# Kernel tuning notes

Hardware: AMD Instinct MI355X
Metric: run time of the kernel (lower is better)

Reference implementation:

```python
import jax, jax.numpy as jnp
import numpy as np

N = 50000          # num_nodes
E = 800000         # general (base) edge count
R_BASE = 3         # base relation types
R = 2 * R_BASE + 1 # base + inverse + self-loop relation
D_IN = 64
D_HID = 64
D_OUT = 64


def _glorot(k, shape):
    # xavier_uniform with relu gain, fan over last two dims
    gain = np.sqrt(2.0)
    bound = gain * np.sqrt(6.0 / (shape[-2] + shape[-1]))
    return jax.random.uniform(k, shape, jnp.float32, -bound, bound)


def setup_inputs() -> dict:
    key = jax.random.key(0)
    ks = jax.random.split(key, 6)
    x = jax.random.normal(ks[0], (N, D_IN), dtype=jnp.float32)
    src = jax.random.randint(ks[1], (E,), 0, N)
    dst = jax.random.randint(ks[2], (E,), 0, N)
    et = jax.random.randint(ks[3], (E,), 0, R_BASE)
    nodes = jnp.arange(N)
    # triples = [original edges, inverse edges (type+R_BASE), self-loops (type 2*R_BASE)]
    triples = jnp.concatenate([
        jnp.stack([src, et, dst], axis=1),
        jnp.stack([dst, et + R_BASE, src], axis=1),
        jnp.stack([nodes, jnp.full((N,), 2 * R_BASE), nodes], axis=1),
    ], axis=0).astype(jnp.int64)
    w1 = _glorot(ks[4], (R, D_IN, D_HID))
    w2 = _glorot(ks[5], (R, D_HID, D_OUT))
    b1 = jnp.zeros((D_HID,), jnp.float32)
    b2 = jnp.zeros((D_OUT,), jnp.float32)
    return {"x": x, "w1": w1, "b1": b1, "w2": w2, "b2": b2,
            "triples": triples, "num_nodes": N, "num_edge_types": R}


def _rgcn_layer(x, W, b, triples, num_nodes, num_rels):
    # vertical stacking: sparse adj [R*N, N], entry (r*N+src, dst) = 1, row-normalised
    src, et, dst = triples[:, 0], triples[:, 1], triples[:, 2]
    rows = et * num_nodes + src                     # [T] row index in stacked adj
    counts = jnp.zeros((num_rels * num_nodes,), x.dtype).at[rows].add(1.0)
    vals = 1.0 / counts[rows]                       # per-edge row-normalised weight
    msgs = vals[:, None] * x[dst]                   # [T, d] gathered + scaled messages
    af = jax.ops.segment_sum(msgs, rows, num_segments=num_rels * num_nodes)
    af = af.reshape(num_rels, num_nodes, x.shape[1])  # [R, N, d]
    return jnp.einsum('rio,rni->no', W, af) + b


def reference(x, w1, b1, w2, b2, triples, num_nodes, num_edge_types):
    h = _rgcn_layer(x, w1, b1, triples, num_nodes, num_edge_types)
    h = jax.nn.relu(h)
    out = _rgcn_layer(h, w2, b2, triples, num_nodes, num_edge_types)
    return out
```

## Files before the change

kernel.cpp:

```cpp
#include <hip/hip_runtime.h>
#include <stdint.h>

#define D 64
#define TILE 2048
#define PK 8
#define NBMAX 128
#define BW 512
#define RMAX 8

typedef __attribute__((ext_vector_type(8))) short bf16x8;
typedef __attribute__((ext_vector_type(4))) float f32x4;

__device__ __forceinline__ float bf2f(unsigned short u) {
    union { unsigned int i; float f; } v; v.i = ((unsigned int)u) << 16; return v.f;
}
__device__ __forceinline__ unsigned short f2bf(float f) {
    union { float f; unsigned int i; } v; v.f = f;
    unsigned int x = v.i;
    unsigned int r = (x + 0x7FFFu + ((x >> 16) & 1u)) >> 16;
    return (unsigned short)r;
}
__device__ __forceinline__ float lo_bf(unsigned int u) {
    union { unsigned int i; float f; } v; v.i = u << 16; return v.f;
}
__device__ __forceinline__ float hi_bf(unsigned int u) {
    union { unsigned int i; float f; } v; v.i = u & 0xFFFF0000u; return v.f;
}

__global__ void detect_kernel(const int* __restrict__ t32, int probe, int expect,
                              unsigned int* __restrict__ flag) {
    if (blockIdx.x == 0 && threadIdx.x == 0)
        flag[0] = (t32[probe] == expect) ? 0u : 1u;
}

__global__ void __launch_bounds__(256) binpass_kernel(const unsigned int* __restrict__ t32,
                                                      const unsigned int* __restrict__ flag,
                                                      unsigned int* __restrict__ staging,
                                                      unsigned int* __restrict__ binCnt,
                                                      int M, int NB, int CAP) {
    __shared__ unsigned int sorted[TILE];
    __shared__ unsigned char sortedb[TILE];
    __shared__ unsigned int hist[NBMAX];
    __shared__ unsigned int scan_[NBMAX];
    __shared__ unsigned int cur[NBMAX];
    __shared__ unsigned int gbase[NBMAX];

    int tid = threadIdx.x;
    int tileBase = blockIdx.x * TILE;

    for (int i = tid; i < NBMAX; i += 256) hist[i] = 0;
    __syncthreads();

    bool is64 = flag[0] != 0;
    unsigned int myE[PK];
    unsigned char myB[PK];
    #pragma unroll
    for (int k = 0; k < PK; k++) {
        int e = tileBase + tid * PK + k;
        myB[k] = 0xFF;
        if (e < M) {
            long w = (long)e * 3;
            unsigned int src, et, dst;
            if (is64) { src = t32[2*w]; et = t32[2*(w+1)]; dst = t32[2*(w+2)]; }
            else      { src = t32[w];   et = t32[w+1];     dst = t32[w+2]; }
            unsigned int b = src >> 9;
            unsigned int lsrc = src & (BW - 1);
            myE[k] = (lsrc << 20) | (et << 17) | dst;
            myB[k] = (unsigned char)b;
            atomicAdd(&hist[b], 1u);
        }
    }
    __syncthreads();

    if (tid < NBMAX) scan_[tid] = hist[tid];
    __syncthreads();
    for (int off = 1; off < NBMAX; off <<= 1) {
        unsigned int v = (tid < NBMAX && tid >= off) ? scan_[tid - off] : 0u;
        __syncthreads();
        if (tid < NBMAX) scan_[tid] += v;
        __syncthreads();
    }
    if (tid < NB) {
        gbase[tid] = atomicAdd(&binCnt[tid], hist[tid]);
        cur[tid] = scan_[tid] - hist[tid];
    }
    __syncthreads();

    #pragma unroll
    for (int k = 0; k < PK; k++) {
        if (myB[k] != 0xFF) {
            unsigned int p = atomicAdd(&cur[myB[k]], 1u);
            sorted[p] = myE[k];
            sortedb[p] = myB[k];
        }
    }
    __syncthreads();

    unsigned int total = scan_[NB - 1];
    for (unsigned int i = tid; i < total; i += 256) {
        unsigned int b = sortedb[i];
        unsigned int local = i - (scan_[b] - hist[b]);
        unsigned int slot = gbase[b] + local;
        if (slot < (unsigned int)CAP)
            staging[(size_t)b * CAP + slot] = sorted[i];
    }
}

__global__ void __launch_bounds__(512) buildcsr_kernel(const unsigned int* __restrict__ staging,
                                                       const unsigned int* __restrict__ binCnt,
                                                       unsigned int* __restrict__ offsets,
                                                       uint2* __restrict__ adj,
                                                       int M, int N, int R, int NB, int CAP) {
    __shared__ unsigned int hist7[RMAX * BW];
    __shared__ unsigned int scanbuf[BW];
    __shared__ unsigned int curs[BW];
    __shared__ unsigned int sbase[NBMAX];

    int b = blockIdx.x, tid = threadIdx.x;
    int nodeBase = b * BW;
    int nNodes = N - nodeBase; if (nNodes > BW) nNodes = BW;
    unsigned int cntB = binCnt[b]; if (cntB > (unsigned int)CAP) cntB = CAP;

    for (int i = tid; i < RMAX * BW; i += 512) hist7[i] = 0;
    __syncthreads();

    const unsigned int* st = staging + (size_t)b * CAP;
    for (unsigned int i = tid; i < cntB; i += 512) {
        unsigned int e = st[i];
        unsigned int lsrc = e >> 20, et = (e >> 17) & 7u;
        atomicAdd(&hist7[et * BW + lsrc], 1u);
    }
    __syncthreads();

    unsigned int d = 0;
    for (int r2 = 0; r2 < R; r2++) d += hist7[r2 * BW + tid];
    scanbuf[tid] = d;
    __syncthreads();
    for (int off = 1; off < BW; off <<= 1) {
        unsigned int v = (tid >= off) ? scanbuf[tid - off] : 0u;
        __syncthreads();
        scanbuf[tid] += v;
        __syncthreads();
    }

    if (tid < NBMAX) sbase[tid] = (tid < NB) ? min(binCnt[tid], (unsigned int)CAP) : 0u;
    __syncthreads();
    for (int off = 1; off < NBMAX; off <<= 1) {
        unsigned int v = (tid < NBMAX && tid >= off) ? sbase[tid - off] : 0u;
        __syncthreads();
        if (tid < NBMAX) sbase[tid] += v;
        __syncthreads();
    }
    unsigned int baseB = (b == 0) ? 0u : sbase[b - 1];

    unsigned int nodeStart = baseB + scanbuf[tid] - d;
    if (tid < nNodes) offsets[nodeBase + tid] = nodeStart;
    if (b == NB - 1 && tid == 0) offsets[N] = baseB + cntB;
    curs[tid] = nodeStart;
    __syncthreads();

    for (unsigned int i = tid; i < cntB; i += 512) {
        unsigned int e = st[i];
        unsigned int lsrc = e >> 20, et = (e >> 17) & 7u, dst = e & 0x1FFFFu;
        unsigned int pos = atomicAdd(&curs[lsrc], 1u);
        float val = 1.0f / (float)hist7[et * BW + lsrc];
        uint2 m; m.x = dst * (unsigned int)R + et; m.y = __float_as_uint(val);
        adj[pos] = m;
    }
}

__global__ void convert_kernel(const float* __restrict__ x, unsigned short* __restrict__ xb, int total) {
    int i = (blockIdx.x * blockDim.x + threadIdx.x) * 4;
    if (i + 3 < total) {
        float4 v = *(const float4*)(x + i);
        ushort4 o; o.x = f2bf(v.x); o.y = f2bf(v.y); o.z = f2bf(v.z); o.w = f2bf(v.w);
        *(ushort4*)(xb + i) = o;
    } else {
        for (int j = i; j < total; j++) xb[j] = f2bf(x[j]);
    }
}

__global__ void packw_kernel(const float* __restrict__ W, unsigned short* __restrict__ wpack, int R) {
    int gid = blockIdx.x * blockDim.x + threadIdx.x;
    if (gid >= R * 512) return;
    int lane = gid & 63;
    int c = (gid >> 6) & 3;
    int t = (gid >> 8) & 1;
    int r = gid >> 9;
    int col = c * 16 + (lane & 15);
    int kbase = t * 32 + 8 * (lane >> 4);
    #pragma unroll
    for (int j = 0; j < 8; j++) {
        wpack[(size_t)gid * 8 + j] = f2bf(W[((size_t)r * D + kbase + j) * D + col]);
    }
}

__global__ void __launch_bounds__(256) gemm_mfma_kernel(const unsigned short* __restrict__ xb,
                                                        const unsigned short* __restrict__ wpack,
                                                        unsigned short* __restrict__ y,
                                                        int N, int R, int nchunks) {
    int wid = blockIdx.x * 4 + (threadIdx.x >> 6);
    int lane = threadIdx.x & 63;
    if (wid >= R * nchunks) return;
    int r = wid / nchunks;
    int chunk = wid - r * nchunks;
    int n0 = chunk * 16;

    int arow = n0 + (lane & 15);
    if (arow >= N) arow = N - 1;
    const unsigned short* xr = xb + (size_t)arow * D + 8 * (lane >> 4);
    bf16x8 a0 = *(const bf16x8*)(xr);
    bf16x8 a1 = *(const bf16x8*)(xr + 32);

    const unsigned short* wp = wpack + (size_t)r * 4096 + (size_t)lane * 8;
    f32x4 zero = {0.f, 0.f, 0.f, 0.f};

    int colb = lane & 15;
    int rowbase = n0 + (lane >> 4) * 4;
    #pragma unroll
    for (int c = 0; c < 4; c++) {
        bf16x8 b0 = *(const bf16x8*)(wp + (size_t)(c) * 512);
        bf16x8 b1 = *(const bf16x8*)(wp + (size_t)(4 + c) * 512);
        f32x4 acc = __builtin_amdgcn_mfma_f32_16x16x32_bf16(a0, b0, zero, 0, 0, 0);
        acc       = __builtin_amdgcn_mfma_f32_16x16x32_bf16(a1, b1, acc,  0, 0, 0);
        int col = 16 * c + colb;
        #pragma unroll
        for (int q = 0; q < 4; q++) {
            int row = rowbase + q;
            if (row < N) y[((size_t)row * R + r) * D + col] = f2bf(acc[q]);
        }
    }
}

__global__ void __launch_bounds__(256) gather_kernel(const unsigned short* __restrict__ y,
                                                     const uint2* __restrict__ adj,
                                                     const unsigned int* __restrict__ offsets,
                                                     const float* __restrict__ bias,
                                                     unsigned int* __restrict__ out_bf,
                                                     float* __restrict__ out_f32,
                                                     int N, int totalWaves, int mode) {
    int w = blockIdx.x * 4 + (threadIdx.x >> 6);
    int lane = threadIdx.x & 63;
    int h = lane >> 5;
    int c = lane & 31;
    float2 bl = ((const float2*)bias)[c];

    for (int n = w; n < N; n += totalWaves) {
        int nu = __builtin_amdgcn_readfirstlane(n);
        unsigned int s = offsets[nu], e = offsets[nu + 1];
        float acc0 = 0.f, acc1 = 0.f;
        unsigned int np = (e - s) >> 1;
        #pragma unroll 4
        for (unsigned int it = 0; it < np; ++it) {
            unsigned int eidx = s + 2 * it + h;
            uint2 m = adj[eidx];
            unsigned int u = *(const unsigned int*)(y + (size_t)m.x * D + 2 * c);
            float val = __uint_as_float(m.y);
            acc0 += val * lo_bf(u);
            acc1 += val * hi_bf(u);
        }
        if ((e - s) & 1u) {
            uint2 m = adj[e - 1];
            unsigned int u = *(const unsigned int*)(y + (size_t)m.x * D + 2 * c);
            float val = (h == 0) ? __uint_as_float(m.y) : 0.f;
            acc0 += val * lo_bf(u);
            acc1 += val * hi_bf(u);
        }
        acc0 += __shfl_xor(acc0, 32);
        acc1 += __shfl_xor(acc1, 32);
        if (lane < 32) {
            float o0 = acc0 + bl.x;
            float o1 = acc1 + bl.y;
            if (mode == 0) {
                o0 = fmaxf(o0, 0.f); o1 = fmaxf(o1, 0.f);
                out_bf[(size_t)nu * 32 + c] =
                    ((unsigned int)f2bf(o1) << 16) | (unsigned int)f2bf(o0);
            } else {
                ((float2*)out_f32)[(size_t)nu * 32 + c] = make_float2(o0, o1);
            }
        }
    }
}

extern "C" void kernel_launch(void* const* d_in, const int* in_sizes, int n_in,
                              void* d_out, int out_size, void* d_ws, size_t ws_size,
                              hipStream_t stream) {
    const float* x  = (const float*)d_in[0];
    const float* w1 = (const float*)d_in[1];
    const float* b1 = (const float*)d_in[2];
    const float* w2 = (const float*)d_in[3];
    const float* b2 = (const float*)d_in[4];
    const int* trip = (const int*)d_in[5];

    const int N = in_sizes[0] / D;
    const int R = in_sizes[1] / (D * D);
    const int M = in_sizes[5] / 3;

    const int NB = (N + BW - 1) / BW;
    const int CAP = (((2 * (M / NB)) + 1023) / 1024) * 1024;

    char* p = (char*)d_ws;
    auto alloc = [&](size_t bytes) { void* q = (void*)p; p += (bytes + 255) / 256 * 256; return q; };
    unsigned int* binCnt  = (unsigned int*)alloc((size_t)NBMAX * 4);
    unsigned int* offsets = (unsigned int*)alloc(((size_t)N + 1) * 4);
    unsigned int* flag    = (unsigned int*)alloc(256);
    unsigned int* staging = (unsigned int*)alloc((size_t)NB * CAP * 4);
    uint2*        adj     = (uint2*)alloc((size_t)M * 8);
    unsigned short* ybf   = (unsigned short*)alloc((size_t)N * R * D * 2);
    unsigned short* xb    = (unsigned short*)alloc((size_t)N * D * 2);
    unsigned short* hb    = (unsigned short*)alloc((size_t)N * D * 2);
    unsigned short* wp1   = (unsigned short*)alloc((size_t)R * 512 * 8 * 2);
    unsigned short* wp2   = (unsigned short*)alloc((size_t)R * 512 * 8 * 2);

    hipMemsetAsync(binCnt, 0, (size_t)NBMAX * 4, stream);

    int probe = (M - N) * 3 + 1;
    detect_kernel<<<1, 1, 0, stream>>>(trip, probe, R - 1, flag);

    int tiles = (M + TILE - 1) / TILE;
    binpass_kernel<<<tiles, 256, 0, stream>>>((const unsigned int*)trip, flag, staging, binCnt, M, NB, CAP);
    buildcsr_kernel<<<NB, 512, 0, stream>>>(staging, binCnt, offsets, adj, M, N, R, NB, CAP);

    int totX = N * D;
    convert_kernel<<<(totX / 4 + 255) / 256, 256, 0, stream>>>(x, xb, totX);
    packw_kernel<<<(R * 512 + 255) / 256, 256, 0, stream>>>(w1, wp1, R);
    packw_kernel<<<(R * 512 + 255) / 256, 256, 0, stream>>>(w2, wp2, R);

    int nchunks = (N + 15) / 16;
    int gb = (R * nchunks + 3) / 4;
    int gblocks = 2048, tw = gblocks * 4;

    gemm_mfma_kernel<<<gb, 256, 0, stream>>>(xb, wp1, ybf, N, R, nchunks);
    gather_kernel<<<gblocks, 256, 0, stream>>>(ybf, adj, offsets, b1, (unsigned int*)hb, nullptr, N, tw, 0);
    gemm_mfma_kernel<<<gb, 256, 0, stream>>>(hb, wp2, ybf, N, R, nchunks);
    gather_kernel<<<gblocks, 256, 0, stream>>>(ybf, adj, offsets, b2, nullptr, (float*)d_out, N, tw, 1);
}
```

Baseline: 272.8 us.

## Aggregate per relation first, then apply a single concatenated-K MFMA GEMM

Reorders each layer from transform-then-gather to aggregate-then-transform. The CSR is now segmented per node and relation, and a new agg kernel gathers raw 64-wide bf16 features into a per-relation concatenated buffer. The self-loop relation is served straight from the feature table. A fused GEMM with K=448 then applies all relation weights, bias and ReLU at once. This removes the N×R×64 intermediate write and the gather from that larger table, in exchange for serial per-relation segment loops with small segments, a wider afcat write and reread, and higher register use in the GEMM.

```diff
diff --git a/kernel.cpp b/kernel.cpp
--- a/kernel.cpp
+++ b/kernel.cpp
@@ -11,9 +11,6 @@
 typedef __attribute__((ext_vector_type(8))) short bf16x8;
 typedef __attribute__((ext_vector_type(4))) float f32x4;
 
-__device__ __forceinline__ float bf2f(unsigned short u) {
-    union { unsigned int i; float f; } v; v.i = ((unsigned int)u) << 16; return v.f;
-}
 __device__ __forceinline__ unsigned short f2bf(float f) {
     union { float f; unsigned int i; } v; v.f = f;
     unsigned int x = v.i;
@@ -108,12 +105,12 @@
 
 __global__ void __launch_bounds__(512) buildcsr_kernel(const unsigned int* __restrict__ staging,
                                                        const unsigned int* __restrict__ binCnt,
-                                                       unsigned int* __restrict__ offsets,
+                                                       unsigned int* __restrict__ segOff,
                                                        uint2* __restrict__ adj,
                                                        int M, int N, int R, int NB, int CAP) {
     __shared__ unsigned int hist7[RMAX * BW];
+    __shared__ unsigned int curs7[RMAX * BW];
     __shared__ unsigned int scanbuf[BW];
-    __shared__ unsigned int curs[BW];
     __shared__ unsigned int sbase[NBMAX];
 
     int b = blockIdx.x, tid = threadIdx.x;
@@ -154,17 +151,25 @@
     unsigned int baseB = (b == 0) ? 0u : sbase[b - 1];
 
     unsigned int nodeStart = baseB + scanbuf[tid] - d;
-    if (tid < nNodes) offsets[nodeBase + tid] = nodeStart;
-    if (b == NB - 1 && tid == 0) offsets[N] = baseB + cntB;
-    curs[tid] = nodeStart;
+    if (tid < nNodes) {
+        unsigned int o = nodeStart;
+        for (int et = 0; et < R; et++) {
+            segOff[(size_t)(nodeBase + tid) * 8 + et] = o;
+            curs7[et * BW + tid] = o;
+            o += hist7[et * BW + tid];
+        }
+        segOff[(size_t)(nodeBase + tid) * 8 + R] = o;
+    } else {
+        for (int et = 0; et < R; et++) curs7[et * BW + tid] = 0;
+    }
     __syncthreads();
 
     for (unsigned int i = tid; i < cntB; i += 512) {
         unsigned int e = st[i];
         unsigned int lsrc = e >> 20, et = (e >> 17) & 7u, dst = e & 0x1FFFFu;
-        unsigned int pos = atomicAdd(&curs[lsrc], 1u);
+        unsigned int pos = atomicAdd(&curs7[et * BW + lsrc], 1u);
         float val = 1.0f / (float)hist7[et * BW + lsrc];
-        uint2 m; m.x = dst * (unsigned int)R + et; m.y = __float_as_uint(val);
+        uint2 m; m.x = dst; m.y = __float_as_uint(val);
         adj[pos] = m;
     }
 }
@@ -195,88 +200,90 @@
     }
 }
 
-__global__ void __launch_bounds__(256) gemm_mfma_kernel(const unsigned short* __restrict__ xb,
-                                                        const unsigned short* __restrict__ wpack,
-                                                        unsigned short* __restrict__ y,
-                                                        int N, int R, int nchunks) {
-    int wid = blockIdx.x * 4 + (threadIdx.x >> 6);
-    int lane = threadIdx.x & 63;
-    if (wid >= R * nchunks) return;
-    int r = wid / nchunks;
-    int chunk = wid - r * nchunks;
-    int n0 = chunk * 16;
-
-    int arow = n0 + (lane & 15);
-    if (arow >= N) arow = N - 1;
-    const unsigned short* xr = xb + (size_t)arow * D + 8 * (lane >> 4);
-    bf16x8 a0 = *(const bf16x8*)(xr);
-    bf16x8 a1 = *(const bf16x8*)(xr + 32);
-
-    const unsigned short* wp = wpack + (size_t)r * 4096 + (size_t)lane * 8;
-    f32x4 zero = {0.f, 0.f, 0.f, 0.f};
-
-    int colb = lane & 15;
-    int rowbase = n0 + (lane >> 4) * 4;
-    #pragma unroll
-    for (int c = 0; c < 4; c++) {
-        bf16x8 b0 = *(const bf16x8*)(wp + (size_t)(c) * 512);
-        bf16x8 b1 = *(const bf16x8*)(wp + (size_t)(4 + c) * 512);
-        f32x4 acc = __builtin_amdgcn_mfma_f32_16x16x32_bf16(a0, b0, zero, 0, 0, 0);
-        acc       = __builtin_amdgcn_mfma_f32_16x16x32_bf16(a1, b1, acc,  0, 0, 0);
-        int col = 16 * c + colb;
-        #pragma unroll
-        for (int q = 0; q < 4; q++) {
-            int row = rowbase + q;
-            if (row < N) y[((size_t)row * R + r) * D + col] = f2bf(acc[q]);
-        }
-    }
-}
-
-__global__ void __launch_bounds__(256) gather_kernel(const unsigned short* __restrict__ y,
-                                                     const uint2* __restrict__ adj,
-                                                     const unsigned int* __restrict__ offsets,
-                                                     const float* __restrict__ bias,
-                                                     unsigned int* __restrict__ out_bf,
-                                                     float* __restrict__ out_f32,
-                                                     int N, int totalWaves, int mode) {
+__global__ void __launch_bounds__(256) agg_kernel(const unsigned short* __restrict__ xtab,
+                                                  const uint2* __restrict__ adj,
+                                                  const unsigned int* __restrict__ segOff,
+                                                  unsigned int* __restrict__ afcat,
+                                                  int N, int totalWaves, int Rm1) {
     int w = blockIdx.x * 4 + (threadIdx.x >> 6);
     int lane = threadIdx.x & 63;
     int h = lane >> 5;
     int c = lane & 31;
-    float2 bl = ((const float2*)bias)[c];
+    int stride = Rm1 * 32;
 
     for (int n = w; n < N; n += totalWaves) {
         int nu = __builtin_amdgcn_readfirstlane(n);
-        unsigned int s = offsets[nu], e = offsets[nu + 1];
-        float acc0 = 0.f, acc1 = 0.f;
-        unsigned int np = (e - s) >> 1;
-        #pragma unroll 4
-        for (unsigned int it = 0; it < np; ++it) {
-            unsigned int eidx = s + 2 * it + h;
-            uint2 m = adj[eidx];
-            unsigned int u = *(const unsigned int*)(y + (size_t)m.x * D + 2 * c);
-            float val = __uint_as_float(m.y);
-            acc0 += val * lo_bf(u);
-            acc1 += val * hi_bf(u);
-        }
-        if ((e - s) & 1u) {
-            uint2 m = adj[e - 1];
-            unsigned int u = *(const unsigned int*)(y + (size_t)m.x * D + 2 * c);
-            float val = (h == 0) ? __uint_as_float(m.y) : 0.f;
-            acc0 += val * lo_bf(u);
-            acc1 += val * hi_bf(u);
-        }
-        acc0 += __shfl_xor(acc0, 32);
-        acc1 += __shfl_xor(acc1, 32);
-        if (lane < 32) {
-            float o0 = acc0 + bl.x;
-            float o1 = acc1 + bl.y;
-            if (mode == 0) {
-                o0 = fmaxf(o0, 0.f); o1 = fmaxf(o1, 0.f);
-                out_bf[(size_t)nu * 32 + c] =
-                    ((unsigned int)f2bf(o1) << 16) | (unsigned int)f2bf(o0);
-            } else {
-                ((float2*)out_f32)[(size_t)nu * 32 + c] = make_float2(o0, o1);
+        for (int r = 0; r < Rm1; r++) {
+            unsigned int s = segOff[(size_t)nu * 8 + r], e = segOff[(size_t)nu * 8 + r + 1];
+            float acc0 = 0.f, acc1 = 0.f;
+            unsigned int cnt = e - s;
+            unsigned int np = cnt >> 1;
+            for (unsigned int it = 0; it < np; ++it) {
+                uint2 m = adj[s + 2 * it + h];
+                unsigned int u = *(const unsigned int*)(xtab + (size_t)m.x * D + 2 * c);
+                float val = __uint_as_float(m.y);
+                acc0 += val * lo_bf(u);
+                acc1 += val * hi_bf(u);
+            }
+            if (cnt & 1u) {
+                uint2 m = adj[e - 1];
+                unsigned int u = *(const unsigned int*)(xtab + (size_t)m.x * D + 2 * c);
+                float val = (h == 0) ? __uint_as_float(m.y) : 0.f;
+                acc0 += val * lo_bf(u);
+                acc1 += val * hi_bf(u);
+            }
+            acc0 += __shfl_xor(acc0, 32);
+            acc1 += __shfl_xor(acc1, 32);
+            if (lane < 32)
+                afcat[(size_t)nu * stride + r * 32 + c] =
+                    ((unsigned int)f2bf(acc1) << 16) | (unsigned int)f2bf(acc0);
+        }
+    }
+}
+
+__global__ void __launch_bounds__(256) gemm2_kernel(const unsigned short* __restrict__ afcat,
+                                                    const unsigned short* __restrict__ xtab,
+                                                    const unsigned short* __restrict__ wpack,
+                                                    const float* __restrict__ bias,
+                                                    unsigned short* __restrict__ out_bf,
+                                                    float* __restrict__ out_f32,
+                                                    int N, int nchunks, int mode) {
+    int wid = blockIdx.x * 4 + (threadIdx.x >> 6);
+    int lane = threadIdx.x & 63;
+    if (wid >= nchunks) return;
+    int n0 = wid * 16;
+    int arow = n0 + (lane & 15);
+    if (arow >= N) arow = N - 1;
+    int ksub = 8 * (lane >> 4);
+
+    bf16x8 a[14];
+    const unsigned short* af = afcat + (size_t)arow * 384 + ksub;
+    #pragma unroll
+    for (int kt = 0; kt < 12; kt++) a[kt] = *(const bf16x8*)(af + kt * 32);
+    const unsigned short* xr = xtab + (size_t)arow * D + ksub;
+    a[12] = *(const bf16x8*)(xr);
+    a[13] = *(const bf16x8*)(xr + 32);
+
+    const unsigned short* wp = wpack + (size_t)lane * 8;
+    int colb = lane & 15;
+    int rowbase = n0 + (lane >> 4) * 4;
+    #pragma unroll
+    for (int c = 0; c < 4; c++) {
+        f32x4 acc = {0.f, 0.f, 0.f, 0.f};
+        #pragma unroll
+        for (int kt = 0; kt < 14; kt++) {
+            bf16x8 bfr = *(const bf16x8*)(wp + (size_t)(kt * 4 + c) * 512);
+            acc = __builtin_amdgcn_mfma_f32_16x16x32_bf16(a[kt], bfr, acc, 0, 0, 0);
+        }
+        int col = 16 * c + colb;
+        float bl = bias[col];
+        #pragma unroll
+        for (int q = 0; q < 4; q++) {
+            int row = rowbase + q;
+            if (row < N) {
+                float o = acc[q] + bl;
+                if (mode == 0) out_bf[(size_t)row * D + col] = f2bf(fmaxf(o, 0.f));
+                else           out_f32[(size_t)row * D + col] = o;
             }
         }
     }
@@ -302,11 +309,11 @@
     char* p = (char*)d_ws;
     auto alloc = [&](size_t bytes) { void* q = (void*)p; p += (bytes + 255) / 256 * 256; return q; };
     unsigned int* binCnt  = (unsigned int*)alloc((size_t)NBMAX * 4);
-    unsigned int* offsets = (unsigned int*)alloc(((size_t)N + 1) * 4);
+    unsigned int* segOff  = (unsigned int*)alloc((size_t)N * 8 * 4);
     unsigned int* flag    = (unsigned int*)alloc(256);
     unsigned int* staging = (unsigned int*)alloc((size_t)NB * CAP * 4);
     uint2*        adj     = (uint2*)alloc((size_t)M * 8);
-    unsigned short* ybf   = (unsigned short*)alloc((size_t)N * R * D * 2);
+    unsigned int* afcat   = (unsigned int*)alloc((size_t)N * (R - 1) * 32 * 4);
     unsigned short* xb    = (unsigned short*)alloc((size_t)N * D * 2);
     unsigned short* hb    = (unsigned short*)alloc((size_t)N * D * 2);
     unsigned short* wp1   = (unsigned short*)alloc((size_t)R * 512 * 8 * 2);
@@ -319,19 +326,19 @@
 
     int tiles = (M + TILE - 1) / TILE;
     binpass_kernel<<<tiles, 256, 0, stream>>>((const unsigned int*)trip, flag, staging, binCnt, M, NB, CAP);
-    buildcsr_kernel<<<NB, 512, 0, stream>>>(staging, binCnt, offsets, adj, M, N, R, NB, CAP);
+    buildcsr_kernel<<<NB, 512, 0, stream>>>(staging, binCnt, segOff, adj, M, N, R, NB, CAP);
 
     int totX = N * D;
     convert_kernel<<<(totX / 4 + 255) / 256, 256, 0, stream>>>(x, xb, totX);
     packw_kernel<<<(R * 512 + 255) / 256, 256, 0, stream>>>(w1, wp1, R);
     packw_kernel<<<(R * 512 + 255) / 256, 256, 0, stream>>>(w2, wp2, R);
 
+    int gblocks = 2048, tw = gblocks * 4;
     int nchunks = (N + 15) / 16;
-    int gb = (R * nchunks + 3) / 4;
-    int gblocks = 2048, tw = gblocks * 4;
-
-    gemm_mfma_kernel<<<gb, 256, 0, stream>>>(xb, wp1, ybf, N, R, nchunks);
-    gather_kernel<<<gblocks, 256, 0, stream>>>(ybf, adj, offsets, b1, (unsigned int*)hb, nullptr, N, tw, 0);
-    gemm_mfma_kernel<<<gb, 256, 0, stream>>>(hb, wp2, ybf, N, R, nchunks);
-    gather_kernel<<<gblocks, 256, 0, stream>>>(ybf, adj, offsets, b2, nullptr, (float*)d_out, N, tw, 1);
-}
+    int gemmb = (nchunks + 3) / 4;
+
+    agg_kernel<<<gblocks, 256, 0, stream>>>(xb, adj, segOff, afcat, N, tw, R - 1);
+    gemm2_kernel<<<gemmb, 256, 0, stream>>>((const unsigned short*)afcat, xb, wp1, b1, hb, nullptr, N, nchunks, 0);
+    agg_kernel<<<gblocks, 256, 0, stream>>>(hb, adj, segOff, afcat, N, tw, R - 1);
+    gemm2_kernel<<<gemmb, 256, 0, stream>>>((const unsigned short*)afcat, hb, wp2, b2, nullptr, (float*)d_out, N, nchunks, 1);
+}
```

Result: slower. 350.0 us (+28.3%).
